# Kernel optimization log

Measured on AMD Instinct MI355X. Metric: run time of the kernel, lower is better.

Reference implementation:

```python
import jax, jax.numpy as jnp
import numpy as np

MARGIN = 0.09
SCALE_POS = 2.0
SCALE_NEG = 40.0
EPS = 1e-05
THRESH1 = 0.501
THRESH2 = 0.531


def setup_inputs() -> dict:
    key = jax.random.key(0)
    k1, k2 = jax.random.split(key)
    B, D, N_CLASSES = 4096, 1024, 64
    feats = jax.random.normal(k1, (B, D), dtype=jnp.float32)
    # thresholds in the loss assume cosine-scale similarities -> L2 normalize
    feats = feats / jnp.linalg.norm(feats, axis=1, keepdims=True)
    labels = jax.random.randint(k2, (B,), 0, N_CLASSES, dtype=jnp.int64)
    return {"feats": feats, "labels": labels}


def reference(feats, labels):
    B = feats.shape[0]
    sim = jnp.matmul(feats, feats.T)  # [B, B]
    eq = labels[:, None] == labels[None, :]
    neg_mask = ~eq
    pos_mask = eq & (sim < 1.0 - EPS)  # drops self-similarity (~1)
    # per-row max over negatives; rows with no negatives -> -inf -> no pos survive
    max_neg = jnp.max(jnp.where(neg_mask, sim, -jnp.inf), axis=1)  # [B]
    pos_mask = pos_mask & ((sim - MARGIN) < max_neg[:, None])
    n_pos = jnp.sum(pos_mask, axis=1)
    n_neg = jnp.sum(neg_mask, axis=1)
    pos_sum = jnp.sum(jnp.where(pos_mask, jnp.exp(-SCALE_POS * sim), 0.0), axis=1)
    neg_sum = jnp.sum(jnp.where(neg_mask, jnp.exp(SCALE_NEG * sim), 0.0), axis=1)
    pos_loss = (1.0 / SCALE_POS) * jnp.log(
        (pos_sum + np.exp(-SCALE_POS * THRESH1)) / (n_pos + 1.0))
    neg_loss = (1.0 / SCALE_NEG) * jnp.log(
        (neg_sum + np.exp(SCALE_NEG * THRESH2)) / (n_neg + 1.0))
    per_row = jnp.log(5.33 + jnp.exp(pos_loss + neg_loss))  # [B]
    valid = (n_neg >= 1) & (n_pos >= 1)
    return jnp.sum(jnp.where(valid, per_row, 0.0)) / B
```

## Files before the change

kernel.cpp:

```cpp
#include <hip/hip_runtime.h>
#include <hip/hip_bf16.h>
#include <math.h>

typedef __attribute__((ext_vector_type(8))) short short8;
typedef __attribute__((ext_vector_type(4))) float floatx4;

#define MARGIN_C    0.09f
#define ONE_M_EPS   0.99999f
#define NCLS        64
#define MEMSTRIDE   256

__device__ __forceinline__ unsigned short f2bf(float f) {
    unsigned u = __float_as_uint(f);
    u += 0x7fffu + ((u >> 16) & 1u);
    return (unsigned short)(u >> 16);
}
__device__ __forceinline__ float bf2f(unsigned short v) {
    return __uint_as_float(((unsigned)v) << 16);
}
__device__ __forceinline__ unsigned fkey(float f) {
    unsigned u = __float_as_uint(f);
    return (u >> 31) ? ~u : (u | 0x80000000u);
}
__device__ __forceinline__ float fdec(unsigned k) {
    return __uint_as_float((k >> 31) ? (k & 0x7fffffffu) : ~k);
}
__device__ __forceinline__ void gld16(const void* g, void* l) {
    __builtin_amdgcn_global_load_lds(
        (const __attribute__((address_space(1))) void*)g,
        (__attribute__((address_space(3))) void*)l, 16, 0, 0);
}

__global__ __launch_bounds__(256) void cvt_build(const float* __restrict__ in,
                                                 unsigned short* __restrict__ out,
                                                 float* __restrict__ statz,
                                                 const int* __restrict__ labels,
                                                 int* __restrict__ members,
                                                 int* __restrict__ classCount,
                                                 float* __restrict__ loss_out,
                                                 int n4, int nz4, int ncvt, int Bn) {
    __shared__ int cnt;
    const int bid = blockIdx.x;
    const int t = threadIdx.x;
    if (bid < ncvt) {
        int i = bid * 256 + t;
        if (bid == 0 && t == 0) loss_out[0] = 0.0f;
        if (i < nz4) ((float4*)statz)[i] = make_float4(0.f, 0.f, 0.f, 0.f);
        if (i >= n4) return;
        float4 v = ((const float4*)in)[i];
        ushort4 o;
        o.x = f2bf(v.x); o.y = f2bf(v.y); o.z = f2bf(v.z); o.w = f2bf(v.w);
        ((ushort4*)out)[i] = o;
    } else {
        const int c = bid - ncvt;
        if (t == 0) cnt = 0;
        __syncthreads();
        for (int j = t; j < Bn; j += 256) {
            if (labels[j] == c) {
                int p = atomicAdd(&cnt, 1);
                if (p < MEMSTRIDE) members[c * MEMSTRIDE + p] = j;
            }
        }
        __syncthreads();
        if (t == 0) classCount[c] = (cnt < MEMSTRIDE) ? cnt : MEMSTRIDE;
    }
}

__global__ __launch_bounds__(256, 2) void gemm_fused(const unsigned short* __restrict__ fb,
                                                     const int* __restrict__ labels,
                                                     float* __restrict__ negsum,
                                                     unsigned* __restrict__ negmax,
                                                     unsigned short* __restrict__ pairsim,
                                                     int Bn, int Dn) {
    __shared__ __align__(16) unsigned short As[2][4096];
    __shared__ __align__(16) unsigned short Bs[2][4096];
    __shared__ int Lrow[128], Lcol[128];

    const int bid = blockIdx.x;
    int by = (int)((sqrtf(8.f * (float)bid + 1.f) - 1.f) * 0.5f);
    while ((by + 1) * (by + 2) / 2 <= bid) by++;
    while (by * (by + 1) / 2 > bid) by--;
    const int bx = bid - by * (by + 1) / 2;
    const bool diag = (bx == by);

    const int t = threadIdx.x;
    const int wave = t >> 6, lane = t & 63;
    const int wr = wave >> 1, wc = wave & 1;
    const int quad = lane >> 4, m16 = lane & 15;

    if (t < 128) Lrow[t] = labels[by * 128 + t];
    else         Lcol[t - 128] = labels[bx * 128 + (t - 128)];

    const int lr = t >> 2, slot = t & 3, kf = (slot + lr) & 3;
    const unsigned short* gA0 = fb + (size_t)(by * 128 + lr) * Dn + kf * 8;
    const unsigned short* gB0 = fb + (size_t)(bx * 128 + lr) * Dn + kf * 8;
    const unsigned short* gA1 = gA0 + (size_t)64 * Dn;
    const unsigned short* gB1 = gB0 + (size_t)64 * Dn;
    const int lb = t * 8;

    floatx4 acc[4][4];
#pragma unroll
    for (int i = 0; i < 4; i++)
#pragma unroll
        for (int j = 0; j < 4; j++) acc[i][j] = (floatx4){0.f, 0.f, 0.f, 0.f};

    const int fragA = (wr * 64 + m16) * 32 + ((quad - m16) & 3) * 8;
    const int fragB = (wc * 64 + m16) * 32 + ((quad - m16) & 3) * 8;

    const int NS = Dn / 32;

    gld16(gA0, &As[0][lb]);
    gld16(gA1, &As[0][2048 + lb]);
    if (!diag) {
        gld16(gB0, &Bs[0][lb]);
        gld16(gB1, &Bs[0][2048 + lb]);
    }
    __syncthreads();

    for (int s = 0; s < NS; s++) {
        if (s + 1 < NS) {
            const int ko = (s + 1) * 32;
            const int nb = (s + 1) & 1;
            gld16(gA0 + ko, &As[nb][lb]);
            gld16(gA1 + ko, &As[nb][2048 + lb]);
            if (!diag) {
                gld16(gB0 + ko, &Bs[nb][lb]);
                gld16(gB1 + ko, &Bs[nb][2048 + lb]);
            }
        }
        __builtin_amdgcn_sched_barrier(0);

        const unsigned short* as_ = As[s & 1];
        const unsigned short* bs_ = diag ? as_ : Bs[s & 1];
        short8 af[4], bfr[4];
#pragma unroll
        for (int i = 0; i < 4; i++) af[i]  = *(const short8*)(as_ + fragA + i * 512);
#pragma unroll
        for (int i = 0; i < 4; i++) bfr[i] = *(const short8*)(bs_ + fragB + i * 512);
#pragma unroll
        for (int i = 0; i < 4; i++)
#pragma unroll
            for (int j = 0; j < 4; j++)
                acc[i][j] = __builtin_amdgcn_mfma_f32_16x16x32_bf16(af[i], bfr[j], acc[i][j], 0, 0, 0);
        __syncthreads();
    }

    const bool offd = !diag;
    int cl[4], gc[4];
#pragma unroll
    for (int j = 0; j < 4; j++) {
        cl[j] = Lcol[wc * 64 + j * 16 + m16];
        gc[j] = bx * 128 + wc * 64 + j * 16 + m16;
    }

    float nsm[4] = {0.f, 0.f, 0.f, 0.f};
    float nmm[4] = {-INFINITY, -INFINITY, -INFINITY, -INFINITY};

#pragma unroll
    for (int i = 0; i < 4; i++) {
#pragma unroll
        for (int r = 0; r < 4; r++) {
            const int rowl = wr * 64 + i * 16 + quad * 4 + r;
            const int rl = Lrow[rowl];
            const int gr = by * 128 + rowl;
            float ns = 0.f, nm = -INFINITY;
#pragma unroll
            for (int j = 0; j < 4; j++) {
                const float s = acc[i][j][r];
                if (cl[j] != rl) {
                    const float e = __expf(40.f * s);
                    ns += e;
                    nm = fmaxf(nm, s);
                    nsm[j] += e;
                    nmm[j] = fmaxf(nmm[j], s);
                } else if ((gr != gc[j]) & (s < ONE_M_EPS)) {
                    const unsigned short v = f2bf(s);
                    pairsim[(size_t)gr * Bn + gc[j]] = v;
                    if (offd) pairsim[(size_t)gc[j] * Bn + gr] = v;
                }
            }
#pragma unroll
            for (int o = 8; o; o >>= 1) {
                ns += __shfl_down(ns, o, 64);
                nm = fmaxf(nm, __shfl_down(nm, o, 64));
            }
            if (m16 == 0) {
                atomicAdd(negsum + gr, ns);
                atomicMax(negmax + gr, fkey(nm));
            }
        }
    }
    if (offd) {
#pragma unroll
        for (int j = 0; j < 4; j++) {
            float v = nsm[j], m = nmm[j];
            v += __shfl_down(v, 16, 64);
            m = fmaxf(m, __shfl_down(m, 16, 64));
            v += __shfl_down(v, 32, 64);
            m = fmaxf(m, __shfl_down(m, 32, 64));
            if (quad == 0) {
                atomicAdd(negsum + gc[j], v);
                atomicMax(negmax + gc[j], fkey(m));
            }
        }
    }
}

__global__ __launch_bounds__(256) void pos_final(const unsigned short* __restrict__ pairsim,
                                                 const int* __restrict__ labels,
                                                 const int* __restrict__ members,
                                                 const int* __restrict__ classCount,
                                                 const unsigned* __restrict__ negmax,
                                                 const float* __restrict__ negsum,
                                                 float* __restrict__ out, int Bn) {
    __shared__ float part[4];
    const int t = threadIdx.x;
    const int wave = t >> 6, lane = t & 63;
    float wacc = 0.f;
#pragma unroll
    for (int rr = 0; rr < 4; rr++) {
        const int r = blockIdx.x * 16 + wave * 4 + rr;
        if (r >= Bn) break;
        const int lab = labels[r];
        const int n = classCount[lab];
        const int base = lab * MEMSTRIDE;
        const float mx = fdec(negmax[r]);
        const unsigned short* prow = pairsim + (size_t)r * Bn;

        float ps = 0.f, pc = 0.f;
        for (int j = lane; j < n; j += 64) {
            const int m = members[base + j];
            if (m != r) {
                const float s = bf2f(prow[m]);
                if ((s - MARGIN_C) < mx) {
                    ps += __expf(-2.f * s);
                    pc += 1.f;
                }
            }
        }
#pragma unroll
        for (int o = 32; o; o >>= 1) {
            ps += __shfl_down(ps, o, 64);
            pc += __shfl_down(pc, o, 64);
        }
        if (lane == 0) {
            const int nneg = Bn - n;
            if (nneg >= 1 && pc >= 0.5f) {
                float pl = 0.5f * logf((ps + expf(-2.f * 0.501f)) / (pc + 1.f));
                float nl = (1.f / 40.f) * logf((negsum[r] + expf(40.f * 0.531f)) / ((float)nneg + 1.f));
                wacc += logf(5.33f + expf(pl + nl));
            }
        }
    }
    if (lane == 0) part[wave] = wacc;
    __syncthreads();
    if (t == 0) {
        atomicAdd(out, (part[0] + part[1] + part[2] + part[3]) / (float)Bn);
    }
}

extern "C" void kernel_launch(void* const* d_in, const int* in_sizes, int n_in,
                              void* d_out, int out_size, void* d_ws, size_t ws_size,
                              hipStream_t stream) {
    const float* feats = (const float*)d_in[0];
    const int* labels  = (const int*)d_in[1];
    float* out = (float*)d_out;

    const int Bn = in_sizes[1];
    const int Dn = in_sizes[0] / Bn;

    unsigned short* fb = (unsigned short*)d_ws;
    float* stats    = (float*)(fb + (size_t)Bn * Dn);
    float* negsum   = stats;
    unsigned* negmax = (unsigned*)(stats + Bn);
    int* classCount = (int*)(stats + 2 * Bn);
    int* members    = classCount + NCLS;
    unsigned short* pairsim = (unsigned short*)(members + NCLS * MEMSTRIDE);

    const int n4   = (Bn * Dn) / 4;
    const int nz4  = (2 * Bn) / 4;
    const int ncvt = (n4 + 255) / 256;
    cvt_build<<<ncvt + NCLS, 256, 0, stream>>>(feats, fb, stats, labels,
                                               members, classCount, out,
                                               n4, nz4, ncvt, Bn);

    const int nt = Bn / 128;
    const int ntri = nt * (nt + 1) / 2;
    gemm_fused<<<ntri, 256, 0, stream>>>(fb, labels, negsum, negmax, pairsim, Bn, Dn);

    pos_final<<<(Bn + 15) / 16, 256, 0, stream>>>(pairsim, labels, members, classCount,
                                                  negmax, negsum, out, Bn);
}
```

Measured before the change: 119.3 us.

## Triple-buffer GEMM K-loop with prefetch depth two and partial vmcnt waits

Switches the fused GEMM main loop from double to triple buffering in LDS. Each step now prefetches two tiles ahead and waits with s_waitcnt vmcnt(4) plus a single barrier, replacing the full __syncthreads after the MFMAs. This lets more global loads stay in flight while compute runs. It also drops the diagonal-tile special case, so diagonal blocks load B redundantly. LDS use grows, and the launch-bounds occupancy hint of 2 is removed.

```diff
diff --git a/kernel.cpp b/kernel.cpp
--- a/kernel.cpp
+++ b/kernel.cpp
@@ -66,14 +66,14 @@
     }
 }
 
-__global__ __launch_bounds__(256, 2) void gemm_fused(const unsigned short* __restrict__ fb,
-                                                     const int* __restrict__ labels,
-                                                     float* __restrict__ negsum,
-                                                     unsigned* __restrict__ negmax,
-                                                     unsigned short* __restrict__ pairsim,
-                                                     int Bn, int Dn) {
-    __shared__ __align__(16) unsigned short As[2][4096];
-    __shared__ __align__(16) unsigned short Bs[2][4096];
+__global__ __launch_bounds__(256) void gemm_fused(const unsigned short* __restrict__ fb,
+                                                  const int* __restrict__ labels,
+                                                  float* __restrict__ negsum,
+                                                  unsigned* __restrict__ negmax,
+                                                  unsigned short* __restrict__ pairsim,
+                                                  int Bn, int Dn) {
+    __shared__ __align__(16) unsigned short As[3][4096];
+    __shared__ __align__(16) unsigned short Bs[3][4096];
     __shared__ int Lrow[128], Lcol[128];
 
     const int bid = blockIdx.x;
@@ -109,29 +109,35 @@
 
     const int NS = Dn / 32;
 
+    __syncthreads();
+
     gld16(gA0, &As[0][lb]);
     gld16(gA1, &As[0][2048 + lb]);
-    if (!diag) {
-        gld16(gB0, &Bs[0][lb]);
-        gld16(gB1, &Bs[0][2048 + lb]);
-    }
-    __syncthreads();
-
+    gld16(gB0, &Bs[0][lb]);
+    gld16(gB1, &Bs[0][2048 + lb]);
+    gld16(gA0 + 32, &As[1][lb]);
+    gld16(gA1 + 32, &As[1][2048 + lb]);
+    gld16(gB0 + 32, &Bs[1][lb]);
+    gld16(gB1 + 32, &Bs[1][2048 + lb]);
+
+    int b = 0, b2 = 2;
     for (int s = 0; s < NS; s++) {
-        if (s + 1 < NS) {
-            const int ko = (s + 1) * 32;
-            const int nb = (s + 1) & 1;
-            gld16(gA0 + ko, &As[nb][lb]);
-            gld16(gA1 + ko, &As[nb][2048 + lb]);
-            if (!diag) {
-                gld16(gB0 + ko, &Bs[nb][lb]);
-                gld16(gB1 + ko, &Bs[nb][2048 + lb]);
-            }
+        if (s == NS - 1) {
+            asm volatile("s_waitcnt vmcnt(0)\n\ts_barrier" ::: "memory");
+        } else {
+            asm volatile("s_waitcnt vmcnt(4)\n\ts_barrier" ::: "memory");
+        }
+        if (s + 2 < NS) {
+            const int ko = (s + 2) * 32;
+            gld16(gA0 + ko, &As[b2][lb]);
+            gld16(gA1 + ko, &As[b2][2048 + lb]);
+            gld16(gB0 + ko, &Bs[b2][lb]);
+            gld16(gB1 + ko, &Bs[b2][2048 + lb]);
         }
         __builtin_amdgcn_sched_barrier(0);
 
-        const unsigned short* as_ = As[s & 1];
-        const unsigned short* bs_ = diag ? as_ : Bs[s & 1];
+        const unsigned short* as_ = &As[b][0];
+        const unsigned short* bs_ = &Bs[b][0];
         short8 af[4], bfr[4];
 #pragma unroll
         for (int i = 0; i < 4; i++) af[i]  = *(const short8*)(as_ + fragA + i * 512);
@@ -142,7 +148,9 @@
 #pragma unroll
             for (int j = 0; j < 4; j++)
                 acc[i][j] = __builtin_amdgcn_mfma_f32_16x16x32_bf16(af[i], bfr[j], acc[i][j], 0, 0, 0);
-        __syncthreads();
+
+        b++;  if (b == 3)  b = 0;
+        b2++; if (b2 == 3) b2 = 0;
     }
 
     const bool offd = !diag;
```

Result: no change. 119.8 us (+0.4%).

## Use single-wave 64x64 GEMM tiles without block barriers

Applied to the files above, without the earlier changes.

Replaces the 256-thread, 128x128-tile triangular GEMM with 64-thread blocks that each compute a 64x64 tile. With only one wave per block, __syncthreads is dropped in favor of an explicit vmcnt wait, and LDS fragment reads are moved ahead of issuing the next stage's async loads. This is meant to remove barrier overhead and raise the number of blocks for better CU occupancy. The cost is less data reuse per tile, so global and L2 traffic roughly doubles, and the triangular grid grows about fourfold.

```diff
diff --git a/kernel.cpp b/kernel.cpp
--- a/kernel.cpp
+++ b/kernel.cpp
@@ -66,15 +66,15 @@
     }
 }
 
-__global__ __launch_bounds__(256, 2) void gemm_fused(const unsigned short* __restrict__ fb,
-                                                     const int* __restrict__ labels,
-                                                     float* __restrict__ negsum,
-                                                     unsigned* __restrict__ negmax,
-                                                     unsigned short* __restrict__ pairsim,
-                                                     int Bn, int Dn) {
-    __shared__ __align__(16) unsigned short As[2][4096];
-    __shared__ __align__(16) unsigned short Bs[2][4096];
-    __shared__ int Lrow[128], Lcol[128];
+__global__ __launch_bounds__(64) void gemm_fused(const unsigned short* __restrict__ fb,
+                                                 const int* __restrict__ labels,
+                                                 float* __restrict__ negsum,
+                                                 unsigned* __restrict__ negmax,
+                                                 unsigned short* __restrict__ pairsim,
+                                                 int Bn, int Dn) {
+    __shared__ __align__(16) unsigned short As[2][2048];
+    __shared__ __align__(16) unsigned short Bs[2][2048];
+    __shared__ int Lrow[64], Lcol[64];
 
     const int bid = blockIdx.x;
     int by = (int)((sqrtf(8.f * (float)bid + 1.f) - 1.f) * 0.5f);
@@ -83,20 +83,17 @@
     const int bx = bid - by * (by + 1) / 2;
     const bool diag = (bx == by);
 
-    const int t = threadIdx.x;
-    const int wave = t >> 6, lane = t & 63;
-    const int wr = wave >> 1, wc = wave & 1;
-    const int quad = lane >> 4, m16 = lane & 15;
-
-    if (t < 128) Lrow[t] = labels[by * 128 + t];
-    else         Lcol[t - 128] = labels[bx * 128 + (t - 128)];
-
-    const int lr = t >> 2, slot = t & 3, kf = (slot + lr) & 3;
-    const unsigned short* gA0 = fb + (size_t)(by * 128 + lr) * Dn + kf * 8;
-    const unsigned short* gB0 = fb + (size_t)(bx * 128 + lr) * Dn + kf * 8;
-    const unsigned short* gA1 = gA0 + (size_t)64 * Dn;
-    const unsigned short* gB1 = gB0 + (size_t)64 * Dn;
-    const int lb = t * 8;
+    const int l = threadIdx.x;
+    const int quad = l >> 4, m16 = l & 15;
+
+    Lrow[l] = labels[by * 64 + l];
+    Lcol[l] = labels[bx * 64 + l];
+
+    const int kf = ((l & 3) + (l >> 2)) & 3;
+    const unsigned short* gA = fb + (size_t)(by * 64 + (l >> 2)) * Dn + kf * 8;
+    const unsigned short* gB = fb + (size_t)(bx * 64 + (l >> 2)) * Dn + kf * 8;
+    const size_t cstep = (size_t)16 * Dn;
+    const int lb = l * 8;
 
     floatx4 acc[4][4];
 #pragma unroll
@@ -104,53 +101,57 @@
 #pragma unroll
         for (int j = 0; j < 4; j++) acc[i][j] = (floatx4){0.f, 0.f, 0.f, 0.f};
 
-    const int fragA = (wr * 64 + m16) * 32 + ((quad - m16) & 3) * 8;
-    const int fragB = (wc * 64 + m16) * 32 + ((quad - m16) & 3) * 8;
-
+    const int fragA = m16 * 32 + ((quad - m16) & 3) * 8;
     const int NS = Dn / 32;
 
-    gld16(gA0, &As[0][lb]);
-    gld16(gA1, &As[0][2048 + lb]);
+    gld16(gA,             &As[0][lb]);
+    gld16(gA + cstep,     &As[0][512 + lb]);
+    gld16(gA + 2 * cstep, &As[0][1024 + lb]);
+    gld16(gA + 3 * cstep, &As[0][1536 + lb]);
     if (!diag) {
-        gld16(gB0, &Bs[0][lb]);
-        gld16(gB1, &Bs[0][2048 + lb]);
-    }
-    __syncthreads();
+        gld16(gB,             &Bs[0][lb]);
+        gld16(gB + cstep,     &Bs[0][512 + lb]);
+        gld16(gB + 2 * cstep, &Bs[0][1024 + lb]);
+        gld16(gB + 3 * cstep, &Bs[0][1536 + lb]);
+    }
 
     for (int s = 0; s < NS; s++) {
+        asm volatile("s_waitcnt vmcnt(0)" ::: "memory");
+        const unsigned short* as_ = &As[s & 1][0];
+        const unsigned short* bs_ = diag ? as_ : &Bs[s & 1][0];
+        short8 af[4], bfr[4];
+#pragma unroll
+        for (int i = 0; i < 4; i++) af[i]  = *(const short8*)(as_ + fragA + i * 512);
+#pragma unroll
+        for (int i = 0; i < 4; i++) bfr[i] = *(const short8*)(bs_ + fragA + i * 512);
+        __builtin_amdgcn_sched_barrier(0);
         if (s + 1 < NS) {
             const int ko = (s + 1) * 32;
             const int nb = (s + 1) & 1;
-            gld16(gA0 + ko, &As[nb][lb]);
-            gld16(gA1 + ko, &As[nb][2048 + lb]);
+            gld16(gA + ko,             &As[nb][lb]);
+            gld16(gA + cstep + ko,     &As[nb][512 + lb]);
+            gld16(gA + 2 * cstep + ko, &As[nb][1024 + lb]);
+            gld16(gA + 3 * cstep + ko, &As[nb][1536 + lb]);
             if (!diag) {
-                gld16(gB0 + ko, &Bs[nb][lb]);
-                gld16(gB1 + ko, &Bs[nb][2048 + lb]);
-            }
-        }
-        __builtin_amdgcn_sched_barrier(0);
-
-        const unsigned short* as_ = As[s & 1];
-        const unsigned short* bs_ = diag ? as_ : Bs[s & 1];
-        short8 af[4], bfr[4];
-#pragma unroll
-        for (int i = 0; i < 4; i++) af[i]  = *(const short8*)(as_ + fragA + i * 512);
-#pragma unroll
-        for (int i = 0; i < 4; i++) bfr[i] = *(const short8*)(bs_ + fragB + i * 512);
+                gld16(gB + ko,             &Bs[nb][lb]);
+                gld16(gB + cstep + ko,     &Bs[nb][512 + lb]);
+                gld16(gB + 2 * cstep + ko, &Bs[nb][1024 + lb]);
+                gld16(gB + 3 * cstep + ko, &Bs[nb][1536 + lb]);
+            }
+        }
 #pragma unroll
         for (int i = 0; i < 4; i++)
 #pragma unroll
             for (int j = 0; j < 4; j++)
                 acc[i][j] = __builtin_amdgcn_mfma_f32_16x16x32_bf16(af[i], bfr[j], acc[i][j], 0, 0, 0);
-        __syncthreads();
     }
 
     const bool offd = !diag;
     int cl[4], gc[4];
 #pragma unroll
     for (int j = 0; j < 4; j++) {
-        cl[j] = Lcol[wc * 64 + j * 16 + m16];
-        gc[j] = bx * 128 + wc * 64 + j * 16 + m16;
+        cl[j] = Lcol[j * 16 + m16];
+        gc[j] = bx * 64 + j * 16 + m16;
     }
 
     float nsm[4] = {0.f, 0.f, 0.f, 0.f};
@@ -160,9 +161,9 @@
     for (int i = 0; i < 4; i++) {
 #pragma unroll
         for (int r = 0; r < 4; r++) {
-            const int rowl = wr * 64 + i * 16 + quad * 4 + r;
+            const int rowl = i * 16 + quad * 4 + r;
             const int rl = Lrow[rowl];
-            const int gr = by * 128 + rowl;
+            const int gr = by * 64 + rowl;
             float ns = 0.f, nm = -INFINITY;
 #pragma unroll
             for (int j = 0; j < 4; j++) {
@@ -284,9 +285,9 @@
                                                members, classCount, out,
                                                n4, nz4, ncvt, Bn);
 
-    const int nt = Bn / 128;
+    const int nt = Bn / 64;
     const int ntri = nt * (nt + 1) / 2;
-    gemm_fused<<<ntri, 256, 0, stream>>>(fb, labels, negsum, negmax, pairsim, Bn, Dn);
+    gemm_fused<<<ntri, 64, 0, stream>>>(fb, labels, negsum, negmax, pairsim, Bn, Dn);
 
     pos_final<<<(Bn + 15) / 16, 256, 0, stream>>>(pairsim, labels, members, classCount,
                                                   negmax, negsum, out, Bn);
```

Measured after the change: 133.6 us. 11.9% more time.

## Deepen GEMM K-step to 64 and pair diagonal tiles per block

Applied to the files above, without the earlier changes.

The K tile of the fused similarity GEMM grows from 32 to 64, so each barrier-separated stage issues twice as many MFMAs, with a wider 8-slot LDS swizzle. Diagonal tiles, which load only one operand, are now packed two per block, so the grid becomes 16 paired-diagonal blocks plus the off-diagonal triangle. The aim is fewer barriers and global-load rounds per tile and better load balance across blocks. Doubling LDS to 64 KB per block may reduce occupancy under the launch bound of 2.

```diff
diff --git a/kernel.cpp b/kernel.cpp
--- a/kernel.cpp
+++ b/kernel.cpp
@@ -72,137 +72,173 @@
                                                      unsigned* __restrict__ negmax,
                                                      unsigned short* __restrict__ pairsim,
                                                      int Bn, int Dn) {
-    __shared__ __align__(16) unsigned short As[2][4096];
-    __shared__ __align__(16) unsigned short Bs[2][4096];
+    __shared__ __align__(16) unsigned short As[2][8192];
+    __shared__ __align__(16) unsigned short Bs[2][8192];
     __shared__ int Lrow[128], Lcol[128];
 
     const int bid = blockIdx.x;
-    int by = (int)((sqrtf(8.f * (float)bid + 1.f) - 1.f) * 0.5f);
-    while ((by + 1) * (by + 2) / 2 <= bid) by++;
-    while (by * (by + 1) / 2 > bid) by--;
-    const int bx = bid - by * (by + 1) / 2;
-    const bool diag = (bx == by);
+    int by, bx, by1 = 0, bx1 = 0, ntl;
+    if (bid < 16) {
+        ntl = 2;
+        by = bx = bid * 2;
+        by1 = bx1 = bid * 2 + 1;
+    } else {
+        ntl = 1;
+        const int m = bid - 16;
+        by = (int)((1.f + sqrtf(8.f * (float)m + 1.f)) * 0.5f);
+        while (by * (by - 1) / 2 > m) by--;
+        while ((by + 1) * by / 2 <= m) by++;
+        bx = m - by * (by - 1) / 2;
+    }
 
     const int t = threadIdx.x;
     const int wave = t >> 6, lane = t & 63;
     const int wr = wave >> 1, wc = wave & 1;
     const int quad = lane >> 4, m16 = lane & 15;
 
-    if (t < 128) Lrow[t] = labels[by * 128 + t];
-    else         Lcol[t - 128] = labels[bx * 128 + (t - 128)];
-
-    const int lr = t >> 2, slot = t & 3, kf = (slot + lr) & 3;
-    const unsigned short* gA0 = fb + (size_t)(by * 128 + lr) * Dn + kf * 8;
-    const unsigned short* gB0 = fb + (size_t)(bx * 128 + lr) * Dn + kf * 8;
-    const unsigned short* gA1 = gA0 + (size_t)64 * Dn;
-    const unsigned short* gB1 = gB0 + (size_t)64 * Dn;
+    const int r0 = t >> 3, kf = (((t & 7) + r0) & 7);
+    const size_t rstep = (size_t)32 * Dn;
     const int lb = t * 8;
 
-    floatx4 acc[4][4];
-#pragma unroll
-    for (int i = 0; i < 4; i++)
-#pragma unroll
-        for (int j = 0; j < 4; j++) acc[i][j] = (floatx4){0.f, 0.f, 0.f, 0.f};
-
-    const int fragA = (wr * 64 + m16) * 32 + ((quad - m16) & 3) * 8;
-    const int fragB = (wc * 64 + m16) * 32 + ((quad - m16) & 3) * 8;
-
-    const int NS = Dn / 32;
-
-    gld16(gA0, &As[0][lb]);
-    gld16(gA1, &As[0][2048 + lb]);
-    if (!diag) {
-        gld16(gB0, &Bs[0][lb]);
-        gld16(gB1, &Bs[0][2048 + lb]);
-    }
-    __syncthreads();
-
-    for (int s = 0; s < NS; s++) {
-        if (s + 1 < NS) {
-            const int ko = (s + 1) * 32;
-            const int nb = (s + 1) & 1;
-            gld16(gA0 + ko, &As[nb][lb]);
-            gld16(gA1 + ko, &As[nb][2048 + lb]);
-            if (!diag) {
-                gld16(gB0 + ko, &Bs[nb][lb]);
-                gld16(gB1 + ko, &Bs[nb][2048 + lb]);
-            }
-        }
-        __builtin_amdgcn_sched_barrier(0);
-
-        const unsigned short* as_ = As[s & 1];
-        const unsigned short* bs_ = diag ? as_ : Bs[s & 1];
-        short8 af[4], bfr[4];
-#pragma unroll
-        for (int i = 0; i < 4; i++) af[i]  = *(const short8*)(as_ + fragA + i * 512);
-#pragma unroll
-        for (int i = 0; i < 4; i++) bfr[i] = *(const short8*)(bs_ + fragB + i * 512);
+    const int fragA = (wr * 64 + m16) * 64;
+    const int fragB = (wc * 64 + m16) * 64;
+    const int sK0 = (quad - m16) & 7;
+    const int sK1 = (quad + 4 - m16) & 7;
+    const int NS = Dn / 64;
+
+    for (int tt = 0; ; tt++) {
+        const bool diag = (bx == by);
+        __syncthreads();
+        if (t < 128) Lrow[t] = labels[by * 128 + t];
+        else         Lcol[t - 128] = labels[bx * 128 + (t - 128)];
+
+        const unsigned short* gA = fb + (size_t)(by * 128 + r0) * Dn + kf * 8;
+        const unsigned short* gB = fb + (size_t)(bx * 128 + r0) * Dn + kf * 8;
+
+        floatx4 acc[4][4];
 #pragma unroll
         for (int i = 0; i < 4; i++)
 #pragma unroll
-            for (int j = 0; j < 4; j++)
-                acc[i][j] = __builtin_amdgcn_mfma_f32_16x16x32_bf16(af[i], bfr[j], acc[i][j], 0, 0, 0);
+            for (int j = 0; j < 4; j++) acc[i][j] = (floatx4){0.f, 0.f, 0.f, 0.f};
+
+        gld16(gA,             &As[0][lb]);
+        gld16(gA + rstep,     &As[0][2048 + lb]);
+        gld16(gA + 2 * rstep, &As[0][4096 + lb]);
+        gld16(gA + 3 * rstep, &As[0][6144 + lb]);
+        if (!diag) {
+            gld16(gB,             &Bs[0][lb]);
+            gld16(gB + rstep,     &Bs[0][2048 + lb]);
+            gld16(gB + 2 * rstep, &Bs[0][4096 + lb]);
+            gld16(gB + 3 * rstep, &Bs[0][6144 + lb]);
+        }
         __syncthreads();
-    }
-
-    const bool offd = !diag;
-    int cl[4], gc[4];
-#pragma unroll
-    for (int j = 0; j < 4; j++) {
-        cl[j] = Lcol[wc * 64 + j * 16 + m16];
-        gc[j] = bx * 128 + wc * 64 + j * 16 + m16;
-    }
-
-    float nsm[4] = {0.f, 0.f, 0.f, 0.f};
-    float nmm[4] = {-INFINITY, -INFINITY, -INFINITY, -INFINITY};
-
-#pragma unroll
-    for (int i = 0; i < 4; i++) {
-#pragma unroll
-        for (int r = 0; r < 4; r++) {
-            const int rowl = wr * 64 + i * 16 + quad * 4 + r;
-            const int rl = Lrow[rowl];
-            const int gr = by * 128 + rowl;
-            float ns = 0.f, nm = -INFINITY;
+
+        for (int s = 0; s < NS; s++) {
+            if (s + 1 < NS) {
+                const int ko = (s + 1) * 64;
+                const int nb = (s + 1) & 1;
+                unsigned short* aw = &As[nb][0];
+                gld16(gA + ko,             aw + lb);
+                gld16(gA + rstep + ko,     aw + 2048 + lb);
+                gld16(gA + 2 * rstep + ko, aw + 4096 + lb);
+                gld16(gA + 3 * rstep + ko, aw + 6144 + lb);
+                if (!diag) {
+                    unsigned short* bw = &Bs[nb][0];
+                    gld16(gB + ko,             bw + lb);
+                    gld16(gB + rstep + ko,     bw + 2048 + lb);
+                    gld16(gB + 2 * rstep + ko, bw + 4096 + lb);
+                    gld16(gB + 3 * rstep + ko, bw + 6144 + lb);
+                }
+            }
+            __builtin_amdgcn_sched_barrier(0);
+
+            const unsigned short* as_ = &As[s & 1][0];
+            const unsigned short* bs_ = diag ? as_ : &Bs[s & 1][0];
+            short8 af[4], bfr[4];
+#pragma unroll
+            for (int i = 0; i < 4; i++) af[i]  = *(const short8*)(as_ + fragA + i * 1024 + sK0 * 8);
+#pragma unroll
+            for (int i = 0; i < 4; i++) bfr[i] = *(const short8*)(bs_ + fragB + i * 1024 + sK0 * 8);
+#pragma unroll
+            for (int i = 0; i < 4; i++)
+#pragma unroll
+                for (int j = 0; j < 4; j++)
+                    acc[i][j] = __builtin_amdgcn_mfma_f32_16x16x32_bf16(af[i], bfr[j], acc[i][j], 0, 0, 0);
+#pragma unroll
+            for (int i = 0; i < 4; i++) af[i]  = *(const short8*)(as_ + fragA + i * 1024 + sK1 * 8);
+#pragma unroll
+            for (int i = 0; i < 4; i++) bfr[i] = *(const short8*)(bs_ + fragB + i * 1024 + sK1 * 8);
+#pragma unroll
+            for (int i = 0; i < 4; i++)
+#pragma unroll
+                for (int j = 0; j < 4; j++)
+                    acc[i][j] = __builtin_amdgcn_mfma_f32_16x16x32_bf16(af[i], bfr[j], acc[i][j], 0, 0, 0);
+
+            __syncthreads();
+        }
+
+        const bool offd = !diag;
+        int cl[4], gc[4];
+#pragma unroll
+        for (int j = 0; j < 4; j++) {
+            cl[j] = Lcol[wc * 64 + j * 16 + m16];
+            gc[j] = bx * 128 + wc * 64 + j * 16 + m16;
+        }
+
+        float nsm[4] = {0.f, 0.f, 0.f, 0.f};
+        float nmm[4] = {-INFINITY, -INFINITY, -INFINITY, -INFINITY};
+
+#pragma unroll
+        for (int i = 0; i < 4; i++) {
+#pragma unroll
+            for (int r = 0; r < 4; r++) {
+                const int rowl = wr * 64 + i * 16 + quad * 4 + r;
+                const int rl = Lrow[rowl];
+                const int gr = by * 128 + rowl;
+                float ns = 0.f, nm = -INFINITY;
+#pragma unroll
+                for (int j = 0; j < 4; j++) {
+                    const float s = acc[i][j][r];
+                    if (cl[j] != rl) {
+                        const float e = __expf(40.f * s);
+                        ns += e;
+                        nm = fmaxf(nm, s);
+                        nsm[j] += e;
+                        nmm[j] = fmaxf(nmm[j], s);
+                    } else if ((gr != gc[j]) & (s < ONE_M_EPS)) {
+                        const unsigned short v = f2bf(s);
+                        pairsim[(size_t)gr * Bn + gc[j]] = v;
+                        if (offd) pairsim[(size_t)gc[j] * Bn + gr] = v;
+                    }
+                }
+#pragma unroll
+                for (int o = 8; o; o >>= 1) {
+                    ns += __shfl_down(ns, o, 64);
+                    nm = fmaxf(nm, __shfl_down(nm, o, 64));
+                }
+                if (m16 == 0) {
+                    atomicAdd(negsum + gr, ns);
+                    atomicMax(negmax + gr, fkey(nm));
+                }
+            }
+        }
+        if (offd) {
 #pragma unroll
             for (int j = 0; j < 4; j++) {
-                const float s = acc[i][j][r];
-                if (cl[j] != rl) {
-                    const float e = __expf(40.f * s);
-                    ns += e;
-                    nm = fmaxf(nm, s);
-                    nsm[j] += e;
-                    nmm[j] = fmaxf(nmm[j], s);
-                } else if ((gr != gc[j]) & (s < ONE_M_EPS)) {
-                    const unsigned short v = f2bf(s);
-                    pairsim[(size_t)gr * Bn + gc[j]] = v;
-                    if (offd) pairsim[(size_t)gc[j] * Bn + gr] = v;
-                }
-            }
-#pragma unroll
-            for (int o = 8; o; o >>= 1) {
-                ns += __shfl_down(ns, o, 64);
-                nm = fmaxf(nm, __shfl_down(nm, o, 64));
-            }
-            if (m16 == 0) {
-                atomicAdd(negsum + gr, ns);
-                atomicMax(negmax + gr, fkey(nm));
-            }
-        }
-    }
-    if (offd) {
-#pragma unroll
-        for (int j = 0; j < 4; j++) {
-            float v = nsm[j], m = nmm[j];
-            v += __shfl_down(v, 16, 64);
-            m = fmaxf(m, __shfl_down(m, 16, 64));
-            v += __shfl_down(v, 32, 64);
-            m = fmaxf(m, __shfl_down(m, 32, 64));
-            if (quad == 0) {
-                atomicAdd(negsum + gc[j], v);
-                atomicMax(negmax + gc[j], fkey(m));
-            }
-        }
+                float v = nsm[j], m = nmm[j];
+                v += __shfl_down(v, 16, 64);
+                m = fmaxf(m, __shfl_down(m, 16, 64));
+                v += __shfl_down(v, 32, 64);
+                m = fmaxf(m, __shfl_down(m, 32, 64));
+                if (quad == 0) {
+                    atomicAdd(negsum + gc[j], v);
+                    atomicMax(negmax + gc[j], fkey(m));
+                }
+            }
+        }
+
+        if (tt + 1 >= ntl) break;
+        by = by1; bx = bx1;
     }
 }
 
@@ -285,8 +321,8 @@
                                                n4, nz4, ncvt, Bn);
 
     const int nt = Bn / 128;
-    const int ntri = nt * (nt + 1) / 2;
-    gemm_fused<<<ntri, 256, 0, stream>>>(fb, labels, negsum, negmax, pairsim, Bn, Dn);
+    const int ngrid = 16 + nt * (nt - 1) / 2;
+    gemm_fused<<<ngrid, 256, 0, stream>>>(fb, labels, negsum, negmax, pairsim, Bn, Dn);
 
     pos_final<<<(Bn + 15) / 16, 256, 0, stream>>>(pairsim, labels, members, classCount,
                                                   negmax, negsum, out, Bn);
```

Result: slower. 128.5 us (+7.7%).
